# Optimization experiments

Measured on AMD Instinct MI355X. Metric: run time of the kernel, lower is better.

The kernel has to match this reference:

```python
import jax, jax.numpy as jnp
import numpy as np

V, D, H, L, B = 30000, 128, 4, 128, 512
HD = D // H  # head dim = 32
NL = 2       # num xLSTM layers


def _layernorm(x, w, b):
    mu = x.mean(-1, keepdims=True)
    var = x.var(-1, keepdims=True)
    return (x - mu) * jax.lax.rsqrt(var + 1e-5) * w + b


def _groupnorm_heads(h, w):
    # GroupNorm with num_groups = H over the channel dim (per-head norm), h: [B,L,D]
    hh = h.reshape(h.shape[0], h.shape[1], H, HD)
    mu = hh.mean(-1, keepdims=True)
    var = hh.var(-1, keepdims=True)
    hh = (hh - mu) * jax.lax.rsqrt(var + 1e-5)
    return hh.reshape(h.shape) * w


def _slstm_block(x, W, R, b, gnw, lnw, lnb):
    # x: [B,L,D]; W: [4,D,D] input gate projections (i,f,z,o); R: [4,H,HD,HD] block-diagonal
    # per-head recurrent weights; b: [4,D]; gnw: [D] groupnorm scale.
    bsz = x.shape[0]
    xn = _layernorm(x, lnw, lnb)
    pre = jnp.einsum('bld,god->lbgo', xn, W) + b  # [L,B,4,D]

    def step(carry, pre_t):
        h, c, n, m = carry  # each [B,D]
        rec = jnp.einsum('bhd,ghde->bghe', h.reshape(bsz, H, HD), R).reshape(bsz, 4, D)
        g = pre_t + rec
        it, ft, zt, ot = g[:, 0], g[:, 1], g[:, 2], g[:, 3]
        # stabilized exponential gating (sLSTM vanilla backend)
        m_new = jnp.maximum(ft + m, it)
        i = jnp.exp(it - m_new)
        f = jnp.exp(ft + m - m_new)
        c_new = f * c + i * jnp.tanh(zt)
        n_new = f * n + i
        h_new = jax.nn.sigmoid(ot) * c_new / n_new
        return (h_new, c_new, n_new, m_new), h_new

    z = jnp.zeros((bsz, D), x.dtype)
    _, hs = jax.lax.scan(step, (z, z, z, z), pre)
    hs = jnp.transpose(hs, (1, 0, 2))  # [B,L,D]
    return x + _groupnorm_heads(hs, gnw)  # residual block


def setup_inputs() -> dict:
    key = jax.random.key(0)
    ks = jax.random.split(key, 10)
    s = lambda k, shape, sc: jax.random.normal(k, shape, jnp.float32) * sc
    return {
        'x_ids': jax.random.randint(ks[0], (B, L), 0, V),
        'emb': s(ks[1], (V, D), 0.02),
        'ln_w': jnp.ones((NL, D), jnp.float32),
        'ln_b': jnp.zeros((NL, D), jnp.float32),
        'Wg': s(ks[2], (NL, 4, D, D), 0.05),
        'Rg': s(ks[3], (NL, 4, H, HD, HD), 0.05),
        'bg': s(ks[4], (NL, 4, D), 0.02),
        'gn_w': jnp.ones((NL, D), jnp.float32),
        'w1': s(ks[5], (64, D), 0.05),
        'b1': jnp.zeros((64,), jnp.float32),
        'w2': s(ks[6], (2, 64), 0.05),
        'b2': jnp.zeros((2,), jnp.float32),
    }


def reference(x_ids, emb, ln_w, ln_b, Wg, Rg, bg, gn_w, w1, b1, w2, b2):
    x = emb[x_ids]  # [B,L,D] embedding lookup
    for l in range(NL):
        x = _slstm_block(x, Wg[l], Rg[l], bg[l], gn_w[l], ln_w[l], ln_b[l])
    pooled = x.mean(axis=1)  # mean over sequence, [B,D]
    hid = jax.nn.relu(pooled @ w1.T + b1)  # dropout is identity at eval
    return hid @ w2.T + b2  # [B,2] logits
```

## Files before the change

kernel.cpp:

```cpp
#include <hip/hip_runtime.h>

typedef _Float16 f16;
typedef unsigned int uint;
typedef f16 f16x2 __attribute__((ext_vector_type(2)));
typedef f16 f16x8 __attribute__((ext_vector_type(8)));
typedef __fp16 h16x2 __attribute__((ext_vector_type(2)));
typedef float f32x4 __attribute__((ext_vector_type(4)));

#define Bn 512
#define Ln 128
#define Dn 128
#define Cn 512

__device__ __forceinline__ float fdot2f(uint a, uint b, float c) {
#if __has_builtin(__builtin_amdgcn_fdot2)
  return __builtin_amdgcn_fdot2(__builtin_bit_cast(f16x2, a),
                                __builtin_bit_cast(f16x2, b), c, false);
#else
  f16x2 av = __builtin_bit_cast(f16x2, a), bv = __builtin_bit_cast(f16x2, b);
  return c + (float)av[0] * (float)bv[0] + (float)av[1] * (float)bv[1];
#endif
}

__device__ __forceinline__ uint pk2(float a, float b) {
#if __has_builtin(__builtin_amdgcn_cvt_pkrtz)
  h16x2 v = __builtin_amdgcn_cvt_pkrtz(a, b);
  return __builtin_bit_cast(uint, v);
#else
  f16x2 v; v[0] = (f16)a; v[1] = (f16)b;
  return __builtin_bit_cast(uint, v);
#endif
}

template<int CTRL>
__device__ __forceinline__ float rorf(float x) {
#if __has_builtin(__builtin_amdgcn_mov_dpp)
  int r = __builtin_amdgcn_mov_dpp(__builtin_bit_cast(int, x), CTRL, 0xF, 0xF, true);
  return __builtin_bit_cast(float, r);
#else
  return __shfl_xor(x, (CTRL - 0x120));
#endif
}

__device__ __forceinline__ int swz16i(float x) {
#if __has_builtin(__builtin_amdgcn_ds_swizzle)
  return __builtin_amdgcn_ds_swizzle(__builtin_bit_cast(int, x), 0x401F);
#else
  return __builtin_bit_cast(int, __shfl_xor(x, 16));
#endif
}

__device__ __forceinline__ void read_hu(const f16* base, uint hu[16]) {
  const uint4* hq = (const uint4*)base;
  uint4 q0 = hq[0], q1 = hq[1], q2 = hq[2], q3 = hq[3];
  hu[0]=q0.x; hu[1]=q0.y; hu[2]=q0.z; hu[3]=q0.w;
  hu[4]=q1.x; hu[5]=q1.y; hu[6]=q1.z; hu[7]=q1.w;
  hu[8]=q2.x; hu[9]=q2.y; hu[10]=q2.z; hu[11]=q2.w;
  hu[12]=q3.x; hu[13]=q3.y; hu[14]=q3.z; hu[15]=q3.w;
}

__global__ __launch_bounds__(256) void k_convert(const float* __restrict__ Wg,
                                                 const float* __restrict__ Rg,
                                                 f16* __restrict__ WhF,
                                                 f16* __restrict__ RT) {
  int i = blockIdx.x * 256 + threadIdx.x;
  const int nWfrag = 2 * 4 * 32 * 64;
  if (i < nWfrag) {
    int lane = i & 63;
    int ii   = (i >> 6) & 31;
    int kk   = (i >> 11) & 3;
    int l    = i >> 13;
    int c = ii * 16 + (lane & 15);
    int d = kk * 32 + ((lane >> 4) << 3);
    const float* src = Wg + ((size_t)(l * 512 + c) * 128 + d);
    f16* dst = WhF + (size_t)i * 8;
    #pragma unroll
    for (int j = 0; j < 8; ++j) dst[j] = (f16)src[j];
  } else {
    int j = i - nWfrag;
    if (j < 32768) {
      int dd = j & 31;
      int e  = (j >> 5) & 31;
      int hh = (j >> 10) & 3;
      int g  = (j >> 12) & 3;
      int l  = j >> 14;
      RT[j] = (f16)Rg[((((l * 4 + g) * 4 + hh) * 32 + dd) * 32) + e];
    }
  }
}

template<int EMB>
__global__ __launch_bounds__(256) void k_gemm(const float* __restrict__ xsrc,
                                              const int* __restrict__ ids,
                                              const float* __restrict__ lw,
                                              const float* __restrict__ lb,
                                              const f16* __restrict__ WhF,
                                              const float* __restrict__ bias,
                                              uint2* __restrict__ preP) {
  int w = threadIdx.x >> 6;
  int lane = threadIdx.x & 63;
  int l16 = lane & 15, quad = lane >> 4;
  int m0 = blockIdx.x * 64 + w * 16;

  const float* src;
  if (EMB) src = xsrc + (size_t)ids[m0 + l16] * Dn;
  else     src = xsrc + (size_t)(m0 + l16) * Dn;
  const float* sp = src + quad * 8;

  f32x4 v[4][2];
  #pragma unroll
  for (int kk = 0; kk < 4; ++kk) {
    v[kk][0] = *(const f32x4*)(sp + kk * 32);
    v[kk][1] = *(const f32x4*)(sp + kk * 32 + 4);
  }
  float s1 = 0.f, s2 = 0.f;
  #pragma unroll
  for (int kk = 0; kk < 4; ++kk)
    #pragma unroll
    for (int p = 0; p < 2; ++p)
      #pragma unroll
      for (int j = 0; j < 4; ++j) {
        float vv = v[kk][p][j];
        s1 += vv; s2 = fmaf(vv, vv, s2);
      }
  s1 += __shfl_xor(s1, 16);  s2 += __shfl_xor(s2, 16);
  s1 += __shfl_xor(s1, 32);  s2 += __shfl_xor(s2, 32);
  float mu = s1 * (1.f / 128.f);
  float var = s2 * (1.f / 128.f) - mu * mu;
  float rs = rsqrtf(var + 1e-5f);

  f16x8 a[4];
  #pragma unroll
  for (int kk = 0; kk < 4; ++kk) {
    #pragma unroll
    for (int p = 0; p < 2; ++p) {
      int d0 = kk * 32 + quad * 8 + p * 4;
      f32x4 lw4 = *(const f32x4*)(lw + d0);
      f32x4 lb4 = *(const f32x4*)(lb + d0);
      #pragma unroll
      for (int j = 0; j < 4; ++j)
        a[kk][p * 4 + j] = (f16)((v[kk][p][j] - mu) * rs * lw4[j] + lb4[j]);
    }
  }

  float bv[32];
  #pragma unroll
  for (int i = 0; i < 32; ++i) bv[i] = bias[i * 16 + l16];

  f32x4 acc[32] = {};
  const f16* bbase = WhF + (size_t)lane * 8;
  #pragma unroll
  for (int kk = 0; kk < 4; ++kk) {
    #pragma unroll
    for (int i = 0; i < 32; ++i) {
      f16x8 bf = *(const f16x8*)(bbase + (size_t)(kk * 32 + i) * 512);
      acc[i] = __builtin_amdgcn_mfma_f32_16x16x32_f16(a[kk], bf, acc[i], 0, 0, 0);
    }
  }
  #pragma unroll
  for (int r = 0; r < 4; ++r) {
    int m = m0 + quad * 4 + r;
    #pragma unroll
    for (int i7 = 0; i7 < 8; ++i7) {
      uint2 vv;
      vv.x = pk2(acc[i7][r]      + bv[i7],      acc[i7 + 8][r]  + bv[i7 + 8]);
      vv.y = pk2(acc[i7 + 16][r] + bv[i7 + 16], acc[i7 + 24][r] + bv[i7 + 24]);
      preP[(size_t)m * Dn + i7 * 16 + l16] = vv;
    }
  }
}

template<int LAST>
__global__ __launch_bounds__(256, 1) void k_scan(const uint2* __restrict__ preP,
                                                 const f16* __restrict__ RT,
                                                 const float* __restrict__ gnw,
                                                 const float* __restrict__ xsrc,
                                                 const int* __restrict__ ids,
                                                 float* __restrict__ xout,
                                                 const float* __restrict__ hw1,
                                                 const float* __restrict__ hb1,
                                                 const float* __restrict__ hw2,
                                                 const float* __restrict__ hb2,
                                                 float* __restrict__ out) {
  const int w = threadIdx.x >> 6;
  const int lane = threadIdx.x & 63;
  const int s = w >> 1;
  const int b = blockIdx.x * 2 + s;
  const int d = ((w & 1) << 6) + lane;
  const int head = d >> 5;
  const int e = d & 31;
  const int half = lane >> 5;

  __shared__ __align__(16) f16 hsh[4][64];
  __shared__ float pool2[2][128];
  __shared__ float hid2[2][64];

  uint rr[4][16];
  const uint* RT32 = (const uint*)RT;
  #pragma unroll
  for (int g = 0; g < 4; ++g) {
    const uint* p = RT32 + ((g * 4 + head) * 32 + e) * 16;
    #pragma unroll
    for (int j = 0; j < 16; ++j) rr[g][j] = p[j];
  }
  const float gw = gnw[d];
  const f16* hbase = &hsh[w][half * 32];

  hsh[w][lane] = (f16)0.f;

  const uint2* pp = preP + (size_t)b * Ln * Dn + d;
  const float* xp = xsrc + (size_t)b * Ln * Dn + d;
  const int*   idr = ids + b * Ln;
  float* xo = xout + (size_t)b * Ln * Dn + d;

  uint2 pb[4]; float xb[4]; int idb[4];
  #pragma unroll
  for (int k = 0; k < 4; ++k) {
    pb[k] = pp[(size_t)k * Dn];
    if (LAST) {
      xb[k] = xp[(size_t)k * Dn];
    } else {
      xb[k] = xsrc[(size_t)idr[k] * Dn + d];
      idb[k] = idr[k + 4];
    }
  }

  uint hu[16];
  read_hu(hbase, hu);

  float cc = 0.f, nc = 0.f, mc = 0.f, psum = 0.f;
  float hprev = 0.f, xprev = 0.f;
  float u1 = 0.f, u2 = 0.f;
  int   w1 = 0,   w2 = 0;

  #pragma unroll 1
  for (int t = 0; t < Ln; t += 4) {
    #pragma unroll
    for (int k = 0; k < 4; ++k) {
      int tt = t + k;
      uint2 pc = pb[k]; float xc = xb[k];
      pb[k] = pp[(size_t)(tt + 4) * Dn];
      if (LAST) {
        xb[k] = xp[(size_t)(tt + 4) * Dn];
      } else {
        xb[k] = xsrc[(size_t)idb[k] * Dn + d];
        int ni = tt + 8;
        idb[k] = idr[ni > 127 ? 127 : ni];
      }

      if (tt > 0) {
        float s1 = u1 + __builtin_bit_cast(float, w1);
        float s2 = u2 + __builtin_bit_cast(float, w2);
        float mu = s1 * (1.f / 32.f);
        float va = s2 * (1.f / 32.f) - mu * mu;
        float ov = xprev + (hprev - mu) * rsqrtf(va + 1e-5f) * gw;
        if (LAST) psum += ov;
        else      xo[(size_t)(tt - 1) * Dn] = ov;
      }

      float a0 = 0.f, a1 = 0.f, a2 = 0.f, a3 = 0.f;
      float c0 = 0.f, c1 = 0.f, c2 = 0.f, c3 = 0.f;
      #pragma unroll
      for (int j = 0; j < 8; ++j) {
        a0 = fdot2f(hu[j], rr[0][j], a0);
        a1 = fdot2f(hu[j], rr[1][j], a1);
        a2 = fdot2f(hu[j], rr[2][j], a2);
        a3 = fdot2f(hu[j], rr[3][j], a3);
        c0 = fdot2f(hu[j + 8], rr[0][j + 8], c0);
        c1 = fdot2f(hu[j + 8], rr[1][j + 8], c1);
        c2 = fdot2f(hu[j + 8], rr[2][j + 8], c2);
        c3 = fdot2f(hu[j + 8], rr[3][j + 8], c3);
      }
      f16x2 lo = __builtin_bit_cast(f16x2, pc.x);
      f16x2 hi = __builtin_bit_cast(f16x2, pc.y);
      float it = ((float)lo[0] + a0) + c0;
      float ft = ((float)lo[1] + a1) + c1;
      float zt = ((float)hi[0] + a2) + c2;
      float ot = ((float)hi[1] + a3) + c3;

      float mn = fmaxf(ft + mc, it);
      float iv = __expf(it - mn);
      float fv = __expf(ft + mc - mn);
      float zc = fminf(fmaxf(zt, -15.f), 15.f);
      float ez = __expf(2.f * zc);
      float tz = (ez - 1.f) * __builtin_amdgcn_rcpf(ez + 1.f);
      float cn = fv * cc + iv * tz;
      float nn = fv * nc + iv;
      float hn = cn * __builtin_amdgcn_rcpf((1.f + __expf(-ot)) * nn);
      cc = cn; nc = nn; mc = mn;

      hsh[w][lane] = (f16)hn;

      float t1v = hn, t2v = hn * hn;
      t1v += rorf<0x121>(t1v);  t2v += rorf<0x121>(t2v);
      t1v += rorf<0x122>(t1v);  t2v += rorf<0x122>(t2v);
      t1v += rorf<0x124>(t1v);  t2v += rorf<0x124>(t2v);
      t1v += rorf<0x128>(t1v);  t2v += rorf<0x128>(t2v);
      w1 = swz16i(t1v);
      w2 = swz16i(t2v);
      u1 = t1v; u2 = t2v;

      read_hu(hbase, hu);

      hprev = hn; xprev = xc;
    }
  }

  {
    float s1 = u1 + __builtin_bit_cast(float, w1);
    float s2 = u2 + __builtin_bit_cast(float, w2);
    float mu = s1 * (1.f / 32.f);
    float va = s2 * (1.f / 32.f) - mu * mu;
    float ov = xprev + (hprev - mu) * rsqrtf(va + 1e-5f) * gw;
    if (LAST) {
      psum += ov;
      pool2[s][d] = psum * (1.f / 128.f);
      __syncthreads();
      if ((w & 1) == 0) {
        int sq = w >> 1;
        float acc = hb1[lane];
        const float* wr = hw1 + (size_t)lane * Dn;
        const float* pl = &pool2[sq][0];
        #pragma unroll 8
        for (int dd = 0; dd < Dn; dd += 4) {
          f32x4 wv = *(const f32x4*)(wr + dd);
          acc += wv[0]*pl[dd] + wv[1]*pl[dd+1] + wv[2]*pl[dd+2] + wv[3]*pl[dd+3];
        }
        hid2[sq][lane] = fmaxf(acc, 0.f);
      }
      __syncthreads();
      if ((w & 1) == 0 && lane < 2) {
        int sq = w >> 1;
        float acc = hb2[lane];
        const float* wr = hw2 + lane * 64;
        #pragma unroll 4
        for (int j = 0; j < 64; ++j) acc += hid2[sq][j] * wr[j];
        out[(blockIdx.x * 2 + sq) * 2 + lane] = acc;
      }
    } else {
      xo[(size_t)(Ln - 1) * Dn] = ov;
    }
  }
}

extern "C" void kernel_launch(void* const* d_in, const int* in_sizes, int n_in,
                              void* d_out, int out_size, void* d_ws, size_t ws_size,
                              hipStream_t stream) {
  const int*   ids  = (const int*)d_in[0];
  const float* emb  = (const float*)d_in[1];
  const float* ln_w = (const float*)d_in[2];
  const float* ln_b = (const float*)d_in[3];
  const float* Wg   = (const float*)d_in[4];
  const float* Rg   = (const float*)d_in[5];
  const float* bg   = (const float*)d_in[6];
  const float* gn_w = (const float*)d_in[7];
  const float* w1   = (const float*)d_in[8];
  const float* b1   = (const float*)d_in[9];
  const float* w2   = (const float*)d_in[10];
  const float* b2   = (const float*)d_in[11];
  float* out = (float*)d_out;

  char* ws = (char*)d_ws;
  uint2* preP = (uint2*)ws;
  float* x1   = (float*)(ws + 67108864);
  f16*   WhF  = (f16*)(ws + 100663296);
  f16*   RT   = (f16*)(ws + 100663296 + 262144);

  k_convert<<<192, 256, 0, stream>>>(Wg, Rg, WhF, RT);

  k_gemm<1><<<1024, 256, 0, stream>>>(emb, ids, ln_w, ln_b, WhF, bg, preP);
  k_scan<0><<<256, 256, 0, stream>>>(preP, RT, gn_w, emb, ids, x1,
                                     nullptr, nullptr, nullptr, nullptr, nullptr);
  k_gemm<0><<<1024, 256, 0, stream>>>(x1, nullptr, ln_w + Dn, ln_b + Dn,
                                      WhF + 65536, bg + Cn, preP);
  k_scan<1><<<256, 256, 0, stream>>>(preP, RT + 16384, gn_w + Dn, x1, nullptr,
                                     nullptr, w1, b1, w2, b2, out);
}
```

Before: 269.9 us.

## Keep GEMM weight fragments in registers and split output columns across waves

Each wave in k_gemm now holds a fixed slice of weight columns (8 N-tiles over all K) in registers, loaded once per block. It then loops over 8 row tiles of 16, so the block covers 128 rows and the grid is halved. Previously every wave streamed the full weight matrix from global/L2 for each 16-row tile. The cost is that each wave now recomputes the layernorm of every row tile it processes, 4x redundantly across the waves, and occupancy is limited by __launch_bounds__(256,2).

```diff
diff --git a/kernel.cpp b/kernel.cpp
--- a/kernel.cpp
+++ b/kernel.cpp
@@ -90,82 +90,103 @@
 }
 
 template<int EMB>
-__global__ __launch_bounds__(256) void k_gemm(const float* __restrict__ xsrc,
-                                              const int* __restrict__ ids,
-                                              const float* __restrict__ lw,
-                                              const float* __restrict__ lb,
-                                              const f16* __restrict__ WhF,
-                                              const float* __restrict__ bias,
-                                              uint2* __restrict__ preP) {
+__global__ __launch_bounds__(256, 2) void k_gemm(const float* __restrict__ xsrc,
+                                                 const int* __restrict__ ids,
+                                                 const float* __restrict__ lw,
+                                                 const float* __restrict__ lb,
+                                                 const f16* __restrict__ WhF,
+                                                 const float* __restrict__ bias,
+                                                 uint2* __restrict__ preP) {
   int w = threadIdx.x >> 6;
   int lane = threadIdx.x & 63;
   int l16 = lane & 15, quad = lane >> 4;
-  int m0 = blockIdx.x * 64 + w * 16;
-
-  const float* src;
-  if (EMB) src = xsrc + (size_t)ids[m0 + l16] * Dn;
-  else     src = xsrc + (size_t)(m0 + l16) * Dn;
-  const float* sp = src + quad * 8;
-
-  f32x4 v[4][2];
-  #pragma unroll
-  for (int kk = 0; kk < 4; ++kk) {
-    v[kk][0] = *(const f32x4*)(sp + kk * 32);
-    v[kk][1] = *(const f32x4*)(sp + kk * 32 + 4);
-  }
-  float s1 = 0.f, s2 = 0.f;
+
+  f16x8 bregs[2][4][4];
+  #pragma unroll
+  for (int j = 0; j < 2; ++j)
+    #pragma unroll
+    for (int g = 0; g < 4; ++g) {
+      int i = 2 * w + j + 8 * g;
+      #pragma unroll
+      for (int kk = 0; kk < 4; ++kk)
+        bregs[j][g][kk] = *(const f16x8*)(WhF + (size_t)(kk * 32 + i) * 512 + lane * 8);
+    }
+  float bv[2][4];
+  #pragma unroll
+  for (int j = 0; j < 2; ++j)
+    #pragma unroll
+    for (int g = 0; g < 4; ++g)
+      bv[j][g] = bias[(2 * w + j + 8 * g) * 16 + l16];
+
+  f32x4 lw4[4][2], lb4[4][2];
   #pragma unroll
   for (int kk = 0; kk < 4; ++kk)
-    #pragma unroll
-    for (int p = 0; p < 2; ++p)
-      #pragma unroll
-      for (int j = 0; j < 4; ++j) {
-        float vv = v[kk][p][j];
-        s1 += vv; s2 = fmaf(vv, vv, s2);
-      }
-  s1 += __shfl_xor(s1, 16);  s2 += __shfl_xor(s2, 16);
-  s1 += __shfl_xor(s1, 32);  s2 += __shfl_xor(s2, 32);
-  float mu = s1 * (1.f / 128.f);
-  float var = s2 * (1.f / 128.f) - mu * mu;
-  float rs = rsqrtf(var + 1e-5f);
-
-  f16x8 a[4];
-  #pragma unroll
-  for (int kk = 0; kk < 4; ++kk) {
     #pragma unroll
     for (int p = 0; p < 2; ++p) {
       int d0 = kk * 32 + quad * 8 + p * 4;
-      f32x4 lw4 = *(const f32x4*)(lw + d0);
-      f32x4 lb4 = *(const f32x4*)(lb + d0);
-      #pragma unroll
-      for (int j = 0; j < 4; ++j)
-        a[kk][p * 4 + j] = (f16)((v[kk][p][j] - mu) * rs * lw4[j] + lb4[j]);
-    }
-  }
-
-  float bv[32];
-  #pragma unroll
-  for (int i = 0; i < 32; ++i) bv[i] = bias[i * 16 + l16];
-
-  f32x4 acc[32] = {};
-  const f16* bbase = WhF + (size_t)lane * 8;
-  #pragma unroll
-  for (int kk = 0; kk < 4; ++kk) {
-    #pragma unroll
-    for (int i = 0; i < 32; ++i) {
-      f16x8 bf = *(const f16x8*)(bbase + (size_t)(kk * 32 + i) * 512);
-      acc[i] = __builtin_amdgcn_mfma_f32_16x16x32_f16(a[kk], bf, acc[i], 0, 0, 0);
-    }
-  }
-  #pragma unroll
-  for (int r = 0; r < 4; ++r) {
-    int m = m0 + quad * 4 + r;
-    #pragma unroll
-    for (int i7 = 0; i7 < 8; ++i7) {
-      uint2 vv;
-      vv.x = pk2(acc[i7][r]      + bv[i7],      acc[i7 + 8][r]  + bv[i7 + 8]);
-      vv.y = pk2(acc[i7 + 16][r] + bv[i7 + 16], acc[i7 + 24][r] + bv[i7 + 24]);
-      preP[(size_t)m * Dn + i7 * 16 + l16] = vv;
+      lw4[kk][p] = *(const f32x4*)(lw + d0);
+      lb4[kk][p] = *(const f32x4*)(lb + d0);
+    }
+
+  #pragma unroll 1
+  for (int t16 = 0; t16 < 8; ++t16) {
+    int m0 = blockIdx.x * 128 + t16 * 16;
+
+    const float* src;
+    if (EMB) src = xsrc + (size_t)ids[m0 + l16] * Dn;
+    else     src = xsrc + (size_t)(m0 + l16) * Dn;
+    const float* sp = src + quad * 8;
+
+    f32x4 v[4][2];
+    #pragma unroll
+    for (int kk = 0; kk < 4; ++kk) {
+      v[kk][0] = *(const f32x4*)(sp + kk * 32);
+      v[kk][1] = *(const f32x4*)(sp + kk * 32 + 4);
+    }
+    float s1 = 0.f, s2 = 0.f;
+    #pragma unroll
+    for (int kk = 0; kk < 4; ++kk)
+      #pragma unroll
+      for (int p = 0; p < 2; ++p)
+        #pragma unroll
+        for (int j = 0; j < 4; ++j) {
+          float vv = v[kk][p][j];
+          s1 += vv; s2 = fmaf(vv, vv, s2);
+        }
+    s1 += __shfl_xor(s1, 16);  s2 += __shfl_xor(s2, 16);
+    s1 += __shfl_xor(s1, 32);  s2 += __shfl_xor(s2, 32);
+    float mu = s1 * (1.f / 128.f);
+    float var = s2 * (1.f / 128.f) - mu * mu;
+    float rs = rsqrtf(var + 1e-5f);
+
+    f16x8 a[4];
+    #pragma unroll
+    for (int kk = 0; kk < 4; ++kk)
+      #pragma unroll
+      for (int p = 0; p < 2; ++p)
+        #pragma unroll
+        for (int j = 0; j < 4; ++j)
+          a[kk][p * 4 + j] = (f16)((v[kk][p][j] - mu) * rs * lw4[kk][p][j] + lb4[kk][p][j]);
+
+    f32x4 acc[2][4] = {};
+    #pragma unroll
+    for (int kk = 0; kk < 4; ++kk)
+      #pragma unroll
+      for (int j = 0; j < 2; ++j)
+        #pragma unroll
+        for (int g = 0; g < 4; ++g)
+          acc[j][g] = __builtin_amdgcn_mfma_f32_16x16x32_f16(a[kk], bregs[j][g][kk], acc[j][g], 0, 0, 0);
+
+    #pragma unroll
+    for (int r = 0; r < 4; ++r) {
+      int m = m0 + quad * 4 + r;
+      #pragma unroll
+      for (int j = 0; j < 2; ++j) {
+        uint2 vv;
+        vv.x = pk2(acc[j][0][r] + bv[j][0], acc[j][1][r] + bv[j][1]);
+        vv.y = pk2(acc[j][2][r] + bv[j][2], acc[j][3][r] + bv[j][3]);
+        preP[(size_t)m * Dn + (2 * w + j) * 16 + l16] = vv;
+      }
     }
   }
 }
@@ -368,11 +389,11 @@
 
   k_convert<<<192, 256, 0, stream>>>(Wg, Rg, WhF, RT);
 
-  k_gemm<1><<<1024, 256, 0, stream>>>(emb, ids, ln_w, ln_b, WhF, bg, preP);
+  k_gemm<1><<<512, 256, 0, stream>>>(emb, ids, ln_w, ln_b, WhF, bg, preP);
   k_scan<0><<<256, 256, 0, stream>>>(preP, RT, gn_w, emb, ids, x1,
                                      nullptr, nullptr, nullptr, nullptr, nullptr);
-  k_gemm<0><<<1024, 256, 0, stream>>>(x1, nullptr, ln_w + Dn, ln_b + Dn,
-                                      WhF + 65536, bg + Cn, preP);
+  k_gemm<0><<<512, 256, 0, stream>>>(x1, nullptr, ln_w + Dn, ln_b + Dn,
+                                     WhF + 65536, bg + Cn, preP);
   k_scan<1><<<256, 256, 0, stream>>>(preP, RT + 16384, gn_w + Dn, x1, nullptr,
                                      nullptr, w1, b1, w2, b2, out);
 }
```

After: 229.0 us (median of 2 runs). -15.2%, faster.
